# Kernel optimization log

Measured on AMD Instinct MI355X. Metric: run time of the kernel, lower is better.

Reference implementation:

```python
import jax, jax.numpy as jnp
import numpy as np

N_HEADS = 16
N_KV_HEADS = 4
N_EMBD = 1024

def setup_inputs() -> dict:
    key = jax.random.key(0)
    kx, kq, kk, kv, ko = jax.random.split(key, 5)
    B, S, E = 2, 2048, N_EMBD
    head_dim = E // N_HEADS
    kv_dim = N_KV_HEADS * head_dim  # 256
    scale = 0.02
    return {
        "x": jax.random.normal(kx, (B, S, E), dtype=jnp.float32),
        "Wq": jax.random.normal(kq, (E, E), dtype=jnp.float32) * scale,
        "Wk": jax.random.normal(kk, (E, kv_dim), dtype=jnp.float32) * scale,
        "Wv": jax.random.normal(kv, (E, kv_dim), dtype=jnp.float32) * scale,
        "Wo": jax.random.normal(ko, (E, E), dtype=jnp.float32) * scale,
    }

def reference(x, Wq, Wk, Wv, Wo):
    B, S, E = x.shape
    H, KV = N_HEADS, N_KV_HEADS
    D = E // H            # head_dim = 64
    R = H // KV           # query heads per kv head = 4
    inv_sqrt_d = 1.0 / (D ** 0.5)

    q = (x @ Wq).reshape(B, S, KV, R, D)   # group query heads by kv group
    k = (x @ Wk).reshape(B, S, KV, D)
    v = (x @ Wv).reshape(B, S, KV, D)

    # repeat_interleave(kv, R, dim=heads) == broadcast kv head g to query heads (g, r)
    scores = jnp.einsum('bqgrd,bkgd->bgrqk', q, k) * inv_sqrt_d  # [B,KV,R,S,S]
    causal = jnp.tril(jnp.ones((S, S), dtype=bool))
    scores = jnp.where(causal, scores, jnp.float32(-jnp.inf))
    attn = jax.nn.softmax(scores, axis=-1)

    out = jnp.einsum('bgrqk,bkgd->bqgrd', attn, v).reshape(B, S, E)
    return out @ Wo
```

## Files before the change

kernel.cpp:

```cpp
#include <hip/hip_runtime.h>
#include <hip/hip_bf16.h>

#define B_SZ   2
#define S_LEN  2048
#define E_DIM  1024
#define H_Q    16
#define H_KV   4
#define HD     64
#define KV_DIM 256
#define M_ROWS (B_SZ * S_LEN)
#define N_QT   (S_LEN / 64)

typedef short bf16x4 __attribute__((ext_vector_type(4)));
typedef short bf16x8 __attribute__((ext_vector_type(8)));
typedef float f32x4  __attribute__((ext_vector_type(4)));
typedef unsigned u32x2 __attribute__((ext_vector_type(2)));

#define MFMA16x32(a, b, c) __builtin_amdgcn_mfma_f32_16x16x32_bf16(a, b, c, 0, 0, 0)

#if __has_builtin(__builtin_amdgcn_mfma_f32_16x16x16bf16_1k)
#define MFMA_PV(a, b, c) __builtin_amdgcn_mfma_f32_16x16x16bf16_1k(a, b, c, 0, 0, 0)
#elif __has_builtin(__builtin_amdgcn_mfma_f32_16x16x16_bf16)
#define MFMA_PV(a, b, c) __builtin_amdgcn_mfma_f32_16x16x16_bf16(a, b, c, 0, 0, 0)
#else
static __device__ inline f32x4 mfma_pv_asm(bf16x4 a, bf16x4 b, f32x4 c) {
    asm volatile("v_mfma_f32_16x16x16_bf16 %0, %1, %2, %0"
                 : "+v"(c) : "v"(a), "v"(b));
    return c;
}
#define MFMA_PV(a, b, c) mfma_pv_asm(a, b, c)
#endif

static __device__ __forceinline__ short f32_to_bf16(float f) {
    unsigned u = __builtin_bit_cast(unsigned, f);
    u += 0x7fffu + ((u >> 16) & 1u);
    return (short)(u >> 16);
}

static __device__ __forceinline__ unsigned pack2_trunc(float a, float b) {
    return __builtin_amdgcn_perm(__builtin_bit_cast(unsigned, b),
                                 __builtin_bit_cast(unsigned, a),
                                 0x07060302u);
}

static __device__ __forceinline__ void load_lds16(const short* g, short* l) {
    __builtin_amdgcn_global_load_lds(
        (const __attribute__((address_space(1))) void*)g,
        (__attribute__((address_space(3))) void*)l, 16, 0, 0);
}

__device__ __forceinline__ void transpose_body(const float* __restrict__ W,
                                               short* __restrict__ Wt,
                                               int K, int N, int bx, int by) {
    __shared__ float t[32][33];
    const int n0 = bx * 32, k0 = by * 32;
    const int tx = threadIdx.x & 31, ty = threadIdx.x >> 5;
#pragma unroll
    for (int i = 0; i < 32; i += 8)
        t[ty + i][tx] = W[(long)(k0 + ty + i) * N + n0 + tx];
    __syncthreads();
#pragma unroll
    for (int i = 0; i < 32; i += 8)
        Wt[(long)(n0 + ty + i) * K + k0 + tx] = f32_to_bf16(t[tx][ty + i]);
}

__global__ __launch_bounds__(256)
void prep(const float* __restrict__ x,
          const float* __restrict__ Wq, const float* __restrict__ Wk,
          const float* __restrict__ Wv, const float* __restrict__ Wo,
          short* __restrict__ xbf, short* __restrict__ Wqt,
          short* __restrict__ Wkt, short* __restrict__ Wvt,
          short* __restrict__ Wot) {
    const int bid = blockIdx.x;
    if (bid < 4096) {
        const int i = bid * 256 + threadIdx.x;
        float4 v = ((const float4*)x)[i];
        bf16x4 o;
        o[0] = f32_to_bf16(v.x); o[1] = f32_to_bf16(v.y);
        o[2] = f32_to_bf16(v.z); o[3] = f32_to_bf16(v.w);
        ((bf16x4*)xbf)[i] = o;
    } else if (bid < 5120) {
        const int r = bid - 4096;
        transpose_body(Wq, Wqt, E_DIM, E_DIM, r & 31, r >> 5);
    } else if (bid < 5376) {
        const int r = bid - 5120;
        transpose_body(Wk, Wkt, E_DIM, KV_DIM, r & 7, r >> 3);
    } else if (bid < 5632) {
        const int r = bid - 5376;
        transpose_body(Wv, Wvt, E_DIM, KV_DIM, r & 7, r >> 3);
    } else {
        const int r = bid - 5632;
        transpose_body(Wo, Wot, E_DIM, E_DIM, r & 31, r >> 5);
    }
}

__device__ __forceinline__ void gemm128x64(const short* __restrict__ Ab,
                                           const short* __restrict__ Btb,
                                           int K, short* As, short* Bs,
                                           f32x4 acc[2][4]) {
    const int tid  = threadIdx.x;
    const int wave = tid >> 6;
    const int lane = tid & 63;
    const int lq   = lane & 15;
    const int lg   = lane >> 4;
    const int lrow = lane >> 2;
    const int lkc  = (lane & 3) * 8;

#pragma unroll
    for (int i = 0; i < 2; ++i)
#pragma unroll
        for (int j = 0; j < 4; ++j) acc[i][j] = (f32x4){0.f, 0.f, 0.f, 0.f};

    for (int k0 = 0; k0 < K; k0 += 32) {
        __syncthreads();
#pragma unroll
        for (int it = 0; it < 2; ++it) {
            const int m0 = wave * 32 + it * 16;
            load_lds16(Ab + (size_t)(m0 + lrow) * K + k0 + lkc, As + m0 * 32);
        }
        {
            const int n0 = wave * 16;
            load_lds16(Btb + (size_t)(n0 + lrow) * K + k0 + lkc, Bs + n0 * 32);
        }
        __syncthreads();
        bf16x8 af[2], bfr[4];
#pragma unroll
        for (int i = 0; i < 2; ++i)
            af[i] = *(const bf16x8*)&As[(wave * 32 + i * 16 + lq) * 32 + lg * 8];
#pragma unroll
        for (int j = 0; j < 4; ++j)
            bfr[j] = *(const bf16x8*)&Bs[(j * 16 + lq) * 32 + lg * 8];
#pragma unroll
        for (int i = 0; i < 2; ++i)
#pragma unroll
            for (int j = 0; j < 4; ++j)
                acc[i][j] = MFMA16x32(af[i], bfr[j], acc[i][j]);
    }
}

__global__ __launch_bounds__(256)
void qkv_gemm(const short* __restrict__ xbf,
              const short* __restrict__ Wqt, const short* __restrict__ Wkt,
              const short* __restrict__ Wvt,
              short* __restrict__ Qbf, short* __restrict__ Kbf,
              short* __restrict__ Vtg, float qscale) {
    __shared__ short As[128 * 32];
    __shared__ short Bs[64 * 32];
    const int nb = blockIdx.x;
    const int mb = blockIdx.y;
    const short* Bt;
    if (nb < 16)      Bt = Wqt + (size_t)nb * 64 * E_DIM;
    else if (nb < 20) Bt = Wkt + (size_t)(nb - 16) * 64 * E_DIM;
    else              Bt = Wvt + (size_t)(nb - 20) * 64 * E_DIM;

    f32x4 acc[2][4];
    gemm128x64(xbf + (size_t)mb * 128 * E_DIM, Bt, E_DIM, As, Bs, acc);

    const int lane = threadIdx.x & 63, wave = threadIdx.x >> 6;
    const int lq = lane & 15, lg = lane >> 4;

    if (nb < 20) {
        short* out; int ldc, ncol0; float alpha;
        if (nb < 16) { out = Qbf; ldc = E_DIM; ncol0 = nb * 64; alpha = qscale; }
        else { out = Kbf; ldc = KV_DIM; ncol0 = (nb - 16) * 64; alpha = 1.f; }
#pragma unroll
        for (int i = 0; i < 2; ++i)
#pragma unroll
            for (int r = 0; r < 4; ++r) {
                const size_t row =
                    (size_t)mb * 128 + wave * 32 + i * 16 + lg * 4 + r;
#pragma unroll
                for (int j = 0; j < 4; ++j)
                    out[row * ldc + ncol0 + j * 16 + lq] =
                        f32_to_bf16(acc[i][j][r] * alpha);
            }
    } else {
        const int gg = nb - 20;
#pragma unroll
        for (int i = 0; i < 2; ++i)
#pragma unroll
            for (int r = 0; r < 4; ++r) {
                const int row = mb * 128 + wave * 32 + i * 16 + lg * 4 + r;
                const int bb = row >> 11, s = row & 2047;
#pragma unroll
                for (int j = 0; j < 4; ++j) {
                    const int d = j * 16 + lq;
                    Vtg[((long)(gg * 2 + bb) * HD + d) * S_LEN + s] =
                        f32_to_bf16(acc[i][j][r]);
                }
            }
    }
}

__global__ __launch_bounds__(256)
void gemm_o(const short* __restrict__ Abf, const short* __restrict__ Wot,
            float* __restrict__ C) {
    __shared__ short As[128 * 32];
    __shared__ short Bs[64 * 32];
    const int nb = blockIdx.x;
    const int mb = blockIdx.y;
    f32x4 acc[2][4];
    gemm128x64(Abf + (size_t)mb * 128 * E_DIM,
               Wot + (size_t)nb * 64 * E_DIM, E_DIM, As, Bs, acc);

    const int lane = threadIdx.x & 63, wave = threadIdx.x >> 6;
    const int lq = lane & 15, lg = lane >> 4;
#pragma unroll
    for (int i = 0; i < 2; ++i)
#pragma unroll
        for (int r = 0; r < 4; ++r) {
            const size_t row =
                (size_t)mb * 128 + wave * 32 + i * 16 + lg * 4 + r;
#pragma unroll
            for (int j = 0; j < 4; ++j)
                C[row * E_DIM + nb * 64 + j * 16 + lq] = acc[i][j][r];
        }
}

struct KVregs { bf16x8 k[2], v[2]; };

__device__ __forceinline__ void stage_load(const short*& pK, const short*& pV,
                                           KVregs& kv) {
#pragma unroll
    for (int it = 0; it < 2; ++it) {
        kv.k[it] = *(const bf16x8*)(pK + (size_t)it * 32 * KV_DIM);
        kv.v[it] = *(const bf16x8*)(pV + (size_t)it * 32 * S_LEN);
    }
    pK += (size_t)64 * KV_DIM;
    pV += 64;
}

__device__ __forceinline__ void stage_write(short (*Ks)[72], short (*Vt)[72],
                                            const KVregs& kv) {
    const int tid = threadIdx.x;
#pragma unroll
    for (int it = 0; it < 2; ++it) {
        const int c   = tid + it * 256;
        const int row = c >> 3;
        const int ch  = c & 7;
        *(bf16x8*)&Ks[row][ch * 8] = kv.k[it];
        *(bf16x8*)&Vt[row][ch * 8] = kv.v[it];
    }
}

__global__ __launch_bounds__(256)
void flash_mfma(const short* __restrict__ Qb,
                const short* __restrict__ Kb,
                const short* __restrict__ Vtg,
                float* __restrict__ Op,
                float* __restrict__ Lp) {
    const int pair  = blockIdx.x;
    const int h     = blockIdx.y;
    const int b     = blockIdx.z >> 1;
    const int split = blockIdx.z & 1;
    const int g     = h >> 2;

    const int tid  = threadIdx.x;
    const int wave = tid >> 6;
    const int lane = tid & 63;
    const int lq   = lane & 15;
    const int lg   = lane >> 4;

    __shared__ short Ks[64][72];
    __shared__ short Vt[64][72];

    const bf16x4 ones4 = {(short)0x3F80, (short)0x3F80,
                          (short)0x3F80, (short)0x3F80};

    for (int rep = 0; rep < 2; ++rep) {
        const int qt = rep ? (N_QT - 1 - pair) : pair;
        const int qs = qt * 64;
        const int half = (qt + 1) >> 1;
        const int kt0  = split ? half : 0;
        const int kt1  = split ? qt : half - 1;

        const short* qrow =
            Qb + ((long)(b * S_LEN + qs + wave * 16 + lq)) * E_DIM + h * HD;
        const bf16x8 qf0 = *(const bf16x8*)(qrow + lg * 8);
        const bf16x8 qf1 = *(const bf16x8*)(qrow + 32 + lg * 8);

        f32x4 o[4];
#pragma unroll
        for (int dc = 0; dc < 4; ++dc) o[dc] = (f32x4){0.f, 0.f, 0.f, 0.f};
        f32x4 lsum = (f32x4){0.f, 0.f, 0.f, 0.f};

        const short* pK = Kb +
            ((long)b * S_LEN + (long)kt0 * 64 + (tid >> 3)) * KV_DIM +
            g * HD + (tid & 7) * 8;
        const short* pV = Vtg +
            ((long)(g * 2 + b) * HD + (tid >> 3)) * S_LEN +
            (long)kt0 * 64 + (tid & 7) * 8;

        KVregs kv;
        if (kt0 <= kt1) stage_load(pK, pV, kv);

        for (int kt = kt0; kt <= kt1; ++kt) {
            __syncthreads();
            stage_write(Ks, Vt, kv);
            __syncthreads();
            if (kt < kt1)
                stage_load(pK, pV, kv);

            const int cmax = (kt == qt) ? wave : 3;
            f32x4 s[4];
#pragma unroll
            for (int c = 0; c < 4; ++c) {
                if (c > cmax) continue;
                bf16x8 kf0 = *(const bf16x8*)&Ks[c * 16 + lq][lg * 8];
                bf16x8 kf1 = *(const bf16x8*)&Ks[c * 16 + lq][32 + lg * 8];
                f32x4 acc = (f32x4){0.f, 0.f, 0.f, 0.f};
                acc = MFMA16x32(kf0, qf0, acc);
                acc = MFMA16x32(kf1, qf1, acc);
                s[c] = acc;
            }

            if (kt == qt) {
#pragma unroll
                for (int r = 0; r < 4; ++r)
                    if (lg * 4 + r > lq) s[wave][r] = -INFINITY;
            }

#pragma unroll
            for (int c = 0; c < 4; ++c) {
                if (c > cmax) continue;
#pragma unroll
                for (int r = 0; r < 4; ++r)
                    s[c][r] = __builtin_amdgcn_exp2f(s[c][r]);
            }

#pragma unroll
            for (int c = 0; c < 4; ++c) {
                if (c > cmax) continue;
                u32x2 packed;
                packed[0] = pack2_trunc(s[c][0], s[c][1]);
                packed[1] = pack2_trunc(s[c][2], s[c][3]);
                bf16x4 pa = __builtin_bit_cast(bf16x4, packed);
                lsum = MFMA_PV(pa, ones4, lsum);
#pragma unroll
                for (int dc = 0; dc < 4; ++dc) {
                    bf16x4 vf =
                        *(const bf16x4*)&Vt[dc * 16 + lq][c * 16 + lg * 4];
                    o[dc] = MFMA_PV(pa, vf, o[dc]);
                }
            }
        }

        const long ibase = (long)(split * 2 + b) << 21;
#pragma unroll
        for (int r = 0; r < 4; ++r) {
            const long base = ibase +
                ((long)(qs + wave * 16 + lg * 4 + r)) * E_DIM + h * HD + lq;
#pragma unroll
            for (int dc = 0; dc < 4; ++dc) Op[base + dc * 16] = o[dc][r];
        }
        if (lq == 0) {
#pragma unroll
            for (int r = 0; r < 4; ++r)
                Lp[((split * 2 + b) * H_Q + h) * S_LEN +
                   qs + wave * 16 + lg * 4 + r] = lsum[r];
        }
    }
}

__global__ __launch_bounds__(256)
void merge_o(const float* __restrict__ Op, const float* __restrict__ Lp,
             short* __restrict__ Abf) {
    const long idx4 = (long)blockIdx.x * 256 + threadIdx.x;
    const long e = idx4 * 4;
    const int b  = (int)(e >> 21);
    const long ei = e & ((1L << 21) - 1);
    const int s  = (int)(ei >> 10);
    const int hh = ((int)(ei & 1023)) >> 6;
    const float4 v0 = *(const float4*)(Op + ((long)(0 + b) << 21) + ei);
    const float4 v1 = *(const float4*)(Op + ((long)(2 + b) << 21) + ei);
    const float l = Lp[((0 + b) * H_Q + hh) * S_LEN + s] +
                    Lp[((2 + b) * H_Q + hh) * S_LEN + s];
    const float inv = 1.f / l;
    bf16x4 o;
    o[0] = f32_to_bf16((v0.x + v1.x) * inv);
    o[1] = f32_to_bf16((v0.y + v1.y) * inv);
    o[2] = f32_to_bf16((v0.z + v1.z) * inv);
    o[3] = f32_to_bf16((v0.w + v1.w) * inv);
    *(bf16x4*)(Abf + e) = o;
}

extern "C" void kernel_launch(void* const* d_in, const int* in_sizes, int n_in,
                              void* d_out, int out_size, void* d_ws, size_t ws_size,
                              hipStream_t stream) {
    const float* x  = (const float*)d_in[0];
    const float* Wq = (const float*)d_in[1];
    const float* Wk = (const float*)d_in[2];
    const float* Wv = (const float*)d_in[3];
    const float* Wo = (const float*)d_in[4];
    float* out = (float*)d_out;

    short* xbf = (short*)d_ws;
    short* Wqt = xbf + (size_t)M_ROWS * E_DIM;
    short* Wkt = Wqt + (size_t)E_DIM * E_DIM;
    short* Wvt = Wkt + (size_t)KV_DIM * E_DIM;
    short* Wot = Wvt + (size_t)KV_DIM * E_DIM;
    short* Qbf = Wot + (size_t)E_DIM * E_DIM;
    short* Kbf = Qbf + (size_t)M_ROWS * E_DIM;
    short* Vtg = Kbf + (size_t)M_ROWS * KV_DIM;
    short* Abf = Vtg + (size_t)8 * HD * S_LEN;
    float* Op  = (float*)(Abf + (size_t)M_ROWS * E_DIM);
    float* Lp  = Op + (size_t)4 * S_LEN * E_DIM;

    const float qscale = 0.125f * 1.44269504088896340736f;

    prep<<<dim3(6656), dim3(256), 0, stream>>>(
        x, Wq, Wk, Wv, Wo, xbf, Wqt, Wkt, Wvt, Wot);
    qkv_gemm<<<dim3(24, M_ROWS / 128), dim3(256), 0, stream>>>(
        xbf, Wqt, Wkt, Wvt, Qbf, Kbf, Vtg, qscale);
    flash_mfma<<<dim3(N_QT / 2, H_Q, 4), dim3(256), 0, stream>>>(
        Qbf, Kbf, Vtg, Op, Lp);
    merge_o<<<dim3(M_ROWS * E_DIM / 4 / 256), dim3(256), 0, stream>>>(
        Op, Lp, Abf);
    gemm_o<<<dim3(E_DIM / 64, M_ROWS / 128), dim3(256), 0, stream>>>(
        Abf, Wot, out);
}
```

Before: 172.2 us.

## Enlarge flash-attention query tile to 128 rows with two fragments per wave

Each block now handles a 128-row query tile, and each wave processes two 16-row query fragments per 64-key tile, so every K/V fragment read from LDS is reused by two MFMA chains. Masking is split into a templated masked/unmasked tile routine, so diagonal handling only runs on the last tiles of the range. The KV range is split between the two blocks at the query-tile boundary (0..QT vs QT+1..2QT+1). This halves the number of blocks and LDS stage loads per query row, at the cost of more registers and a grid half the size, which reduces parallelism.

```diff
diff --git a/kernel.cpp b/kernel.cpp
--- a/kernel.cpp
+++ b/kernel.cpp
@@ -9,7 +9,7 @@
 #define HD     64
 #define KV_DIM 256
 #define M_ROWS (B_SZ * S_LEN)
-#define N_QT   (S_LEN / 64)
+#define N_QT128 (S_LEN / 128)
 
 typedef short bf16x4 __attribute__((ext_vector_type(4)));
 typedef short bf16x8 __attribute__((ext_vector_type(8)));
@@ -243,6 +243,75 @@
     }
 }
 
+template <bool MASKED>
+__device__ __forceinline__ void proc_tile(const short (*Ks)[72],
+                                          const short (*Vt)[72],
+                                          const bf16x8 (&qf)[2][2],
+                                          int lq, int lg, int dd,
+                                          f32x4 (&o)[2][4],
+                                          f32x4 (&lsum)[2]) {
+    f32x4 s[4][2];
+    bool need[4][2];
+#pragma unroll
+    for (int c = 0; c < 4; ++c) {
+        const int rel0 = c * 16 - dd;
+        need[c][0] = !MASKED || (rel0 < 16);
+        need[c][1] = !MASKED || (rel0 - 16 < 16);
+        if (MASKED && !need[c][1]) continue;
+        bf16x8 kf0 = *(const bf16x8*)&Ks[c * 16 + lq][lg * 8];
+        bf16x8 kf1 = *(const bf16x8*)&Ks[c * 16 + lq][32 + lg * 8];
+#pragma unroll
+        for (int f = 0; f < 2; ++f) {
+            if (MASKED && !need[c][f]) continue;
+            f32x4 acc = (f32x4){0.f, 0.f, 0.f, 0.f};
+            acc = MFMA16x32(kf0, qf[f][0], acc);
+            acc = MFMA16x32(kf1, qf[f][1], acc);
+            if (MASKED) {
+                if (c * 16 - 16 * f - dd == 0) {
+#pragma unroll
+                    for (int r = 0; r < 4; ++r)
+                        if (lg * 4 + r > lq) acc[r] = -INFINITY;
+                }
+            }
+            s[c][f] = acc;
+        }
+    }
+
+#pragma unroll
+    for (int c = 0; c < 4; ++c)
+#pragma unroll
+        for (int f = 0; f < 2; ++f) {
+            if (MASKED && !need[c][f]) continue;
+#pragma unroll
+            for (int r = 0; r < 4; ++r)
+                s[c][f][r] = __builtin_amdgcn_exp2f(s[c][f][r]);
+        }
+
+    const bf16x4 ones4 = {(short)0x3F80, (short)0x3F80,
+                          (short)0x3F80, (short)0x3F80};
+#pragma unroll
+    for (int c = 0; c < 4; ++c) {
+        if (MASKED && !need[c][1]) continue;
+        bf16x4 pa[2];
+#pragma unroll
+        for (int f = 0; f < 2; ++f) {
+            if (MASKED && !need[c][f]) continue;
+            u32x2 packed;
+            packed[0] = pack2_trunc(s[c][f][0], s[c][f][1]);
+            packed[1] = pack2_trunc(s[c][f][2], s[c][f][3]);
+            pa[f] = __builtin_bit_cast(bf16x4, packed);
+            lsum[f] = MFMA_PV(pa[f], ones4, lsum[f]);
+        }
+#pragma unroll
+        for (int dc = 0; dc < 4; ++dc) {
+            bf16x4 vf = *(const bf16x4*)&Vt[dc * 16 + lq][c * 16 + lg * 4];
+#pragma unroll
+            for (int f = 0; f < 2; ++f)
+                if (!MASKED || need[c][f]) o[f][dc] = MFMA_PV(pa[f], vf, o[f][dc]);
+        }
+    }
+}
+
 __global__ __launch_bounds__(256)
 void flash_mfma(const short* __restrict__ Qb,
                 const short* __restrict__ Kb,
@@ -256,7 +325,7 @@
     const int g     = h >> 2;
 
     const int tid  = threadIdx.x;
-    const int wave = tid >> 6;
+    const int wv   = tid >> 6;
     const int lane = tid & 63;
     const int lq   = lane & 15;
     const int lg   = lane >> 4;
@@ -264,25 +333,30 @@
     __shared__ short Ks[64][72];
     __shared__ short Vt[64][72];
 
-    const bf16x4 ones4 = {(short)0x3F80, (short)0x3F80,
-                          (short)0x3F80, (short)0x3F80};
-
     for (int rep = 0; rep < 2; ++rep) {
-        const int qt = rep ? (N_QT - 1 - pair) : pair;
-        const int qs = qt * 64;
-        const int half = (qt + 1) >> 1;
-        const int kt0  = split ? half : 0;
-        const int kt1  = split ? qt : half - 1;
+        const int QT = rep ? (N_QT128 - 1 - pair) : pair;
+        const int Q0 = QT * 128;
+        const int kt0 = split ? QT + 1 : 0;
+        const int kt1 = split ? 2 * QT + 1 : QT;
+        const int nmask = split ? ((QT >= 1) ? 2 : 1) : ((QT == 0) ? 1 : 0);
+        const int qmin = Q0 + wv * 32;
 
         const short* qrow =
-            Qb + ((long)(b * S_LEN + qs + wave * 16 + lq)) * E_DIM + h * HD;
-        const bf16x8 qf0 = *(const bf16x8*)(qrow + lg * 8);
-        const bf16x8 qf1 = *(const bf16x8*)(qrow + 32 + lg * 8);
-
-        f32x4 o[4];
-#pragma unroll
-        for (int dc = 0; dc < 4; ++dc) o[dc] = (f32x4){0.f, 0.f, 0.f, 0.f};
-        f32x4 lsum = (f32x4){0.f, 0.f, 0.f, 0.f};
+            Qb + ((long)(b * S_LEN + qmin + lq)) * E_DIM + h * HD;
+        bf16x8 qf[2][2];
+#pragma unroll
+        for (int f = 0; f < 2; ++f) {
+            qf[f][0] = *(const bf16x8*)(qrow + (long)f * 16 * E_DIM + lg * 8);
+            qf[f][1] = *(const bf16x8*)(qrow + (long)f * 16 * E_DIM + 32 + lg * 8);
+        }
+
+        f32x4 o[2][4];
+#pragma unroll
+        for (int f = 0; f < 2; ++f)
+#pragma unroll
+            for (int dc = 0; dc < 4; ++dc) o[f][dc] = (f32x4){0.f, 0.f, 0.f, 0.f};
+        f32x4 lsum[2];
+        lsum[0] = lsum[1] = (f32x4){0.f, 0.f, 0.f, 0.f};
 
         const short* pK = Kb +
             ((long)b * S_LEN + (long)kt0 * 64 + (tid >> 3)) * KV_DIM +
@@ -301,63 +375,31 @@
             if (kt < kt1)
                 stage_load(pK, pV, kv);
 
-            const int cmax = (kt == qt) ? wave : 3;
-            f32x4 s[4];
-#pragma unroll
-            for (int c = 0; c < 4; ++c) {
-                if (c > cmax) continue;
-                bf16x8 kf0 = *(const bf16x8*)&Ks[c * 16 + lq][lg * 8];
-                bf16x8 kf1 = *(const bf16x8*)&Ks[c * 16 + lq][32 + lg * 8];
-                f32x4 acc = (f32x4){0.f, 0.f, 0.f, 0.f};
-                acc = MFMA16x32(kf0, qf0, acc);
-                acc = MFMA16x32(kf1, qf1, acc);
-                s[c] = acc;
+            if (kt <= kt1 - nmask) {
+                proc_tile<false>(Ks, Vt, qf, lq, lg, 0, o, lsum);
+            } else {
+                const int dd = __builtin_amdgcn_readfirstlane(qmin - kt * 64);
+                proc_tile<true>(Ks, Vt, qf, lq, lg, dd, o, lsum);
             }
-
-            if (kt == qt) {
+        }
+
+        const long ibase = (long)(split * 2 + b) << 21;
+#pragma unroll
+        for (int f = 0; f < 2; ++f)
+#pragma unroll
+            for (int r = 0; r < 4; ++r) {
+                const long base = ibase +
+                    ((long)(qmin + f * 16 + lg * 4 + r)) * E_DIM + h * HD + lq;
+#pragma unroll
+                for (int dc = 0; dc < 4; ++dc) Op[base + dc * 16] = o[f][dc][r];
+            }
+        if (lq == 0) {
+#pragma unroll
+            for (int f = 0; f < 2; ++f)
 #pragma unroll
                 for (int r = 0; r < 4; ++r)
-                    if (lg * 4 + r > lq) s[wave][r] = -INFINITY;
-            }
-
-#pragma unroll
-            for (int c = 0; c < 4; ++c) {
-                if (c > cmax) continue;
-#pragma unroll
-                for (int r = 0; r < 4; ++r)
-                    s[c][r] = __builtin_amdgcn_exp2f(s[c][r]);
-            }
-
-#pragma unroll
-            for (int c = 0; c < 4; ++c) {
-                if (c > cmax) continue;
-                u32x2 packed;
-                packed[0] = pack2_trunc(s[c][0], s[c][1]);
-                packed[1] = pack2_trunc(s[c][2], s[c][3]);
-                bf16x4 pa = __builtin_bit_cast(bf16x4, packed);
-                lsum = MFMA_PV(pa, ones4, lsum);
-#pragma unroll
-                for (int dc = 0; dc < 4; ++dc) {
-                    bf16x4 vf =
-                        *(const bf16x4*)&Vt[dc * 16 + lq][c * 16 + lg * 4];
-                    o[dc] = MFMA_PV(pa, vf, o[dc]);
-                }
-            }
-        }
-
-        const long ibase = (long)(split * 2 + b) << 21;
-#pragma unroll
-        for (int r = 0; r < 4; ++r) {
-            const long base = ibase +
-                ((long)(qs + wave * 16 + lg * 4 + r)) * E_DIM + h * HD + lq;
-#pragma unroll
-            for (int dc = 0; dc < 4; ++dc) Op[base + dc * 16] = o[dc][r];
-        }
-        if (lq == 0) {
-#pragma unroll
-            for (int r = 0; r < 4; ++r)
-                Lp[((split * 2 + b) * H_Q + h) * S_LEN +
-                   qs + wave * 16 + lg * 4 + r] = lsum[r];
+                    Lp[((split * 2 + b) * H_Q + h) * S_LEN +
+                       qmin + f * 16 + lg * 4 + r] = lsum[f][r];
         }
     }
 }
@@ -412,7 +454,7 @@
         x, Wq, Wk, Wv, Wo, xbf, Wqt, Wkt, Wvt, Wot);
     qkv_gemm<<<dim3(24, M_ROWS / 128), dim3(256), 0, stream>>>(
         xbf, Wqt, Wkt, Wvt, Qbf, Kbf, Vtg, qscale);
-    flash_mfma<<<dim3(N_QT / 2, H_Q, 4), dim3(256), 0, stream>>>(
+    flash_mfma<<<dim3(8, H_Q, 4), dim3(256), 0, stream>>>(
         Qbf, Kbf, Vtg, Op, Lp);
     merge_o<<<dim3(M_ROWS * E_DIM / 4 / 256), dim3(256), 0, stream>>>(
         Op, Lp, Abf);
```

Result: faster. 165.6 us (-3.8%).
